# Kernel optimization log

Hardware: AMD Instinct MI355X
Metric: run time of the kernel (lower is better)

The kernel has to match this reference:

```python
import jax, jax.numpy as jnp
import numpy as np

N = 20000      # nodes
E = 160000     # edges (avg degree 16)
IN_DIM = 256
HID = 128      # hidden_dim == per-head out_channels in PyG TransformerConv
HEADS = 4
EPS = 1e-5


def setup_inputs() -> dict:
    key = jax.random.key(0)
    ks = jax.random.split(key, 24)

    def w(k, shape, scale=0.05):
        return jax.random.normal(k, shape, dtype=jnp.float32) * scale

    inp = {
        "x": jax.random.normal(ks[0], (N, IN_DIM), dtype=jnp.float32),
        "edge_index": jax.random.randint(ks[1], (2, E), 0, N, dtype=jnp.int32),
        # input projection
        "lin_w": w(ks[2], (IN_DIM, HID)), "lin_b": jnp.zeros((HID,), jnp.float32),
    }
    i = 3
    for l in (1, 2):
        inp[f"q_w{l}"] = w(ks[i], (HID, HEADS * HID)); i += 1
        inp[f"q_b{l}"] = jnp.zeros((HEADS * HID,), jnp.float32)
        inp[f"k_w{l}"] = w(ks[i], (HID, HEADS * HID)); i += 1
        inp[f"k_b{l}"] = jnp.zeros((HEADS * HID,), jnp.float32)
        inp[f"v_w{l}"] = w(ks[i], (HID, HEADS * HID)); i += 1
        inp[f"v_b{l}"] = jnp.zeros((HEADS * HID,), jnp.float32)
        inp[f"s_w{l}"] = w(ks[i], (HID, HID)); i += 1
        inp[f"s_b{l}"] = jnp.zeros((HID,), jnp.float32)
        inp[f"ln_g{l}"] = jnp.ones((HID,), jnp.float32)
        inp[f"ln_b{l}"] = jnp.zeros((HID,), jnp.float32)
    return inp


def _segment_softmax(scores, seg, num):
    # scores: [E, HEADS], seg: [E] destination indices
    m = jax.ops.segment_max(scores, seg, num_segments=num)
    m = jnp.where(jnp.isfinite(m), m, 0.0)  # guard empty segments
    e = jnp.exp(scores - m[seg])
    d = jax.ops.segment_sum(e, seg, num_segments=num)
    return e / (d[seg] + 1e-16)


def _transformer_conv(x, src, dst, qw, qb, kw, kb, vw, vb, sw, sb):
    # PyG TransformerConv(HID, HID, heads=HEADS, concat=False)
    n = x.shape[0]
    q = (x @ qw + qb).reshape(n, HEADS, HID)
    k = (x @ kw + kb).reshape(n, HEADS, HID)
    v = (x @ vw + vb).reshape(n, HEADS, HID)
    # per-edge attention: query at dst (i), key/value at src (j)
    alpha = jnp.einsum("ehd,ehd->eh", q[dst], k[src]) / jnp.sqrt(jnp.float32(HID))
    alpha = _segment_softmax(alpha, dst, n)                 # [E, HEADS]
    msg = v[src] * alpha[..., None]                          # [E, HEADS, HID]
    out = jax.ops.segment_sum(msg, dst, num_segments=n)      # [N, HEADS, HID]
    out = out.mean(axis=1)                                   # concat=False -> head mean
    return out + x @ sw + sb                                 # root skip connection


def _layer_norm(x, g, b):
    mu = x.mean(-1, keepdims=True)
    var = ((x - mu) ** 2).mean(-1, keepdims=True)
    return (x - mu) * jax.lax.rsqrt(var + EPS) * g + b


def reference(x, edge_index, lin_w, lin_b,
              q_w1, q_b1, k_w1, k_b1, v_w1, v_b1, s_w1, s_b1, ln_g1, ln_b1,
              q_w2, q_b2, k_w2, k_b2, v_w2, v_b2, s_w2, s_b2, ln_g2, ln_b2):
    src, dst = edge_index[0], edge_index[1]
    h = jax.nn.relu(x @ lin_w + lin_b)
    h1 = _transformer_conv(h, src, dst, q_w1, q_b1, k_w1, k_b1, v_w1, v_b1, s_w1, s_b1)
    h = _layer_norm(h1 + h, ln_g1, ln_b1)
    h2 = _transformer_conv(h, src, dst, q_w2, q_b2, k_w2, k_b2, v_w2, v_b2, s_w2, s_b2)
    h = _layer_norm(h2 + h, ln_g2, ln_b2)
    return h
```

## Files before the change

kernel.cpp:

```cpp
#include <hip/hip_runtime.h>
#include <math.h>

#define NNODE 20000
#define NEDGE 160000
#define IN_DIMV 256
#define HIDV 128
#define DEGCAP 64
#define RING 8

typedef __attribute__((ext_vector_type(8))) short bf16x8;
typedef __attribute__((ext_vector_type(4))) float f32x4;
typedef __attribute__((ext_vector_type(2))) float f32x2;

__device__ __forceinline__ float bf2f(unsigned short u) {
    union { unsigned int i; float f; } x; x.i = ((unsigned int)u) << 16; return x.f;
}
__device__ __forceinline__ unsigned short f2bf(float f) {
    union { float f; unsigned int i; } x; x.f = f;
    unsigned int r = x.i + 0x7fffu + ((x.i >> 16) & 1u);
    return (unsigned short)(r >> 16);
}
__device__ __forceinline__ void unpack8(uint4 p, float* f) {
    f[0] = bf2f((unsigned short)(p.x & 0xffff)); f[1] = bf2f((unsigned short)(p.x >> 16));
    f[2] = bf2f((unsigned short)(p.y & 0xffff)); f[3] = bf2f((unsigned short)(p.y >> 16));
    f[4] = bf2f((unsigned short)(p.z & 0xffff)); f[5] = bf2f((unsigned short)(p.z >> 16));
    f[6] = bf2f((unsigned short)(p.w & 0xffff)); f[7] = bf2f((unsigned short)(p.w >> 16));
}
__device__ __forceinline__ void unpack8f8_w(unsigned int a, unsigned int b, float* f) {
    f32x2 t;
    t = __builtin_amdgcn_cvt_pk_f32_fp8((int)a, false); f[0] = t.x; f[1] = t.y;
    t = __builtin_amdgcn_cvt_pk_f32_fp8((int)a, true);  f[2] = t.x; f[3] = t.y;
    t = __builtin_amdgcn_cvt_pk_f32_fp8((int)b, false); f[4] = t.x; f[5] = t.y;
    t = __builtin_amdgcn_cvt_pk_f32_fp8((int)b, true);  f[6] = t.x; f[7] = t.y;
}
__device__ __forceinline__ unsigned char f2fp8(float v) {
    int pk = __builtin_amdgcn_cvt_pk_fp8_f32(v, v, 0, false);
    return (unsigned char)(pk & 0xff);
}
__device__ __forceinline__ void gld_lds16(const unsigned short* g, unsigned short* l) {
    __builtin_amdgcn_global_load_lds((const __attribute__((address_space(1))) void*)g,
                                     (__attribute__((address_space(3))) void*)l, 16, 0, 0);
}
__device__ __forceinline__ void gld_lds16b(const unsigned char* g, unsigned char* l) {
    __builtin_amdgcn_global_load_lds((const __attribute__((address_space(1))) void*)g,
                                     (__attribute__((address_space(3))) void*)l, 16, 0, 0);
}

__global__ void convert_kernel(
    const float* __restrict__ x, const float* __restrict__ lin_w,
    const float* __restrict__ qw0, const float* __restrict__ kw0,
    const float* __restrict__ vw0, const float* __restrict__ sw0,
    const float* __restrict__ qw1, const float* __restrict__ kw1,
    const float* __restrict__ vw1, const float* __restrict__ sw1,
    unsigned short* __restrict__ xbf, unsigned short* __restrict__ arena)
{
    int idx = blockIdx.x * 256 + threadIdx.x;
    if (idx < 5120000) { xbf[idx] = f2bf(x[idx]); return; }
    int id2 = idx - 5120000;
    if (id2 >= 458752) return;
    float v;
    if (id2 < 32768) {
        int n = id2 >> 8, k = id2 & 255;
        v = lin_w[k * 128 + n];
    } else {
        int t = id2 - 32768;
        int l = t / 212992, r = t % 212992;
        int n = r >> 7, k = r & 127;
        const float* qw = l ? qw1 : qw0;
        const float* kw = l ? kw1 : kw0;
        const float* vw = l ? vw1 : vw0;
        const float* sw = l ? sw1 : sw0;
        if (n < 1536) {
            const float* w = (n < 512) ? qw : (n < 1024) ? kw : vw;
            v = w[k * 512 + (n & 511)];
        } else {
            v = sw[k * 128 + (n - 1536)];
        }
    }
    arena[id2] = f2bf(v);
}

template <int MODE, int K>
__global__ __launch_bounds__(256) void mfma_gemm(
    const unsigned short* __restrict__ A, const unsigned short* __restrict__ WT,
    const float* __restrict__ b0, const float* __restrict__ b1,
    const float* __restrict__ b2, const float* __restrict__ b3,
    unsigned short* __restrict__ qb_out, unsigned char* __restrict__ kv8_out,
    unsigned short* __restrict__ pre16_out, unsigned short* __restrict__ hbf_out)
{
    constexpr bool FULLK = (K == 128);
    __shared__ unsigned short smem[FULLK ? 32768 : 8192];
    unsigned short* ot = smem;
    unsigned char* ot8 = (unsigned char*)smem;

    int tid = threadIdx.x;
    int lane = tid & 63;
    int w = tid >> 6;
    int wm = w & 1, wn = w >> 1;
    int bm = blockIdx.x * 128;
    int bn = blockIdx.y * 128;

    int srow = lane >> 2;
    int scol = (lane & 3) * 8;
    int ar0 = bm + w * 32 + srow;      if (ar0 > NNODE - 1) ar0 = NNODE - 1;
    int ar1 = bm + w * 32 + 16 + srow; if (ar1 > NNODE - 1) ar1 = NNODE - 1;
    int br0 = bn + w * 32 + srow;
    int br1 = bn + w * 32 + 16 + srow;

    f32x4 acc[4][4] = {};
    int arow = wm * 64 + (lane & 15);
    int brow = wn * 64 + (lane & 15);
    int koff = (lane >> 4) * 8;

    if constexpr (FULLK) {
        unsigned short* As = smem;
        unsigned short* Bs = smem + 16384;
#pragma unroll
        for (int c = 0; c < 4; c++) {
            int k0 = c * 32;
            gld_lds16(A + (size_t)ar0 * K + k0 + scol, As + c * 4096 + (w * 32) * 32);
            gld_lds16(A + (size_t)ar1 * K + k0 + scol, As + c * 4096 + (w * 32 + 16) * 32);
            gld_lds16(WT + (size_t)br0 * K + k0 + scol, Bs + c * 4096 + (w * 32) * 32);
            gld_lds16(WT + (size_t)br1 * K + k0 + scol, Bs + c * 4096 + (w * 32 + 16) * 32);
        }
        __syncthreads();
#pragma unroll
        for (int c = 0; c < 4; c++) {
            bf16x8 fa[4], fb[4];
#pragma unroll
            for (int i = 0; i < 4; i++) fa[i] = *(const bf16x8*)&As[c * 4096 + (arow + i * 16) * 32 + koff];
#pragma unroll
            for (int i = 0; i < 4; i++) fb[i] = *(const bf16x8*)&Bs[c * 4096 + (brow + i * 16) * 32 + koff];
#pragma unroll
            for (int mi = 0; mi < 4; mi++)
#pragma unroll
                for (int ni = 0; ni < 4; ni++)
                    acc[mi][ni] = __builtin_amdgcn_mfma_f32_16x16x32_bf16(fa[mi], fb[ni], acc[mi][ni], 0, 0, 0);
        }
    } else {
        unsigned short* As = smem;
        unsigned short* Bs = smem + 4096;
        for (int k0 = 0; k0 < K; k0 += 32) {
            gld_lds16(A + (size_t)ar0 * K + k0 + scol, As + (w * 32) * 32);
            gld_lds16(A + (size_t)ar1 * K + k0 + scol, As + (w * 32 + 16) * 32);
            gld_lds16(WT + (size_t)br0 * K + k0 + scol, Bs + (w * 32) * 32);
            gld_lds16(WT + (size_t)br1 * K + k0 + scol, Bs + (w * 32 + 16) * 32);
            __syncthreads();
            bf16x8 fa[4], fb[4];
#pragma unroll
            for (int i = 0; i < 4; i++) fa[i] = *(const bf16x8*)&As[(arow + i * 16) * 32 + koff];
#pragma unroll
            for (int i = 0; i < 4; i++) fb[i] = *(const bf16x8*)&Bs[(brow + i * 16) * 32 + koff];
#pragma unroll
            for (int mi = 0; mi < 4; mi++)
#pragma unroll
                for (int ni = 0; ni < 4; ni++)
                    acc[mi][ni] = __builtin_amdgcn_mfma_f32_16x16x32_bf16(fa[mi], fb[ni], acc[mi][ni], 0, 0, 0);
            __syncthreads();
        }
    }

    int quad = lane >> 4, lcol = lane & 15;

    if (MODE == 1 && bn >= 512 && bn < 1536) {
        const float* bb = (bn < 1024) ? (b1 + bn - 512) : (b2 + bn - 1024);
        int coff = bn - 512;
#pragma unroll
        for (int hh = 0; hh < 2; hh++) {
            __syncthreads();
            if (wm == hh) {
#pragma unroll
                for (int mi = 0; mi < 4; mi++) {
#pragma unroll
                    for (int ni = 0; ni < 4; ni++) {
                        int lc = wn * 64 + ni * 16 + lcol;
                        float bias = bb[lc];
#pragma unroll
                        for (int reg = 0; reg < 4; reg++) {
                            int lr = mi * 16 + quad * 4 + reg;
                            ot8[lr * 128 + lc] = f2fp8(acc[mi][ni][reg] + bias);
                        }
                    }
                }
            }
            __syncthreads();
            int r = tid >> 2, ch = tid & 3;
            int row = bm + hh * 64 + r;
            if (row < NNODE) {
                uint4* dp = (uint4*)(kv8_out + (size_t)row * 1024 + coff + ch * 32);
                const uint4* sp = (const uint4*)(ot8 + r * 128 + ch * 32);
                dp[0] = sp[0];
                dp[1] = sp[1];
            }
        }
        return;
    }

    unsigned short* dst;
    int dstride, coloff;
    const float* bb;
    if (MODE == 0)           { dst = hbf_out;   dstride = HIDV; coloff = 0;  bb = b0; }
    else if (bn < 512)       { dst = qb_out;    dstride = 512;  coloff = bn; bb = b0 + bn; }
    else                     { dst = pre16_out; dstride = HIDV; coloff = 0;  bb = b3; }

#pragma unroll
    for (int hh = 0; hh < 2; hh++) {
        __syncthreads();
        if (wm == hh) {
#pragma unroll
            for (int mi = 0; mi < 4; mi++) {
#pragma unroll
                for (int ni = 0; ni < 4; ni++) {
                    int lc = wn * 64 + ni * 16 + lcol;
                    float bias = bb[lc];
#pragma unroll
                    for (int reg = 0; reg < 4; reg++) {
                        float v = acc[mi][ni][reg] + bias;
                        if (MODE == 0) v = fmaxf(v, 0.f);
                        ot[(mi * 16 + quad * 4 + reg) * 128 + lc] = f2bf(v);
                    }
                }
            }
        }
        __syncthreads();
        int r = tid >> 2, ch = tid & 3;
        int row = bm + hh * 64 + r;
        if (row < NNODE) {
            uint4* dp = (uint4*)(dst + (size_t)row * dstride + coloff + ch * 32);
            const uint4* sp = (const uint4*)(ot + r * 128 + ch * 32);
#pragma unroll
            for (int q = 0; q < 4; q++) dp[q] = sp[q];
        }
    }
}

__global__ void scatter_kernel(const int* __restrict__ ei, int* __restrict__ cursor,
                               int* __restrict__ bucket) {
    int e = blockIdx.x * blockDim.x + threadIdx.x;
    if (e < NEDGE) {
        int d = ei[NEDGE + e];
        int slot = atomicAdd(&cursor[d], 1);
        if (slot < DEGCAP) bucket[d * DEGCAP + slot] = ei[e];
    }
}

__global__ __launch_bounds__(256) void attn_ln_kernel(
    const unsigned short* __restrict__ qb, const unsigned char* __restrict__ kv8,
    const int* __restrict__ cursor, const int* __restrict__ bucket,
    const unsigned short* __restrict__ pre16, const float* __restrict__ g,
    const float* __restrict__ b,
    unsigned short* __restrict__ hbf ,
    float* __restrict__ extout)
{
    __shared__ __align__(16) unsigned char ring[4][RING * 1024];
    int lane = threadIdx.x & 63;
    int wid = threadIdx.x >> 6;
    int i = blockIdx.x * 4 + wid;
    int cnt = cursor[i]; if (cnt > DEGCAP) cnt = DEGCAP;
    const int* bk = bucket + i * DEGCAP;
    unsigned char* myring = ring[wid];

    int hg = lane >> 4;
    int sl = lane & 15;

    float qr[8];
    {
        uint4 p = *(const uint4*)(qb + (size_t)i * 512 + lane * 8);
        unpack8(p, qr);
#pragma unroll
        for (int j = 0; j < 8; j++) qr[j] *= 0.0883883476483184f;
    }

    float m = -INFINITY, l = 0.f;
    float acc[8] = {0.f, 0.f, 0.f, 0.f, 0.f, 0.f, 0.f, 0.f};

    for (int j0 = 0; j0 < cnt; j0 += RING) {
        int nb = cnt - j0; if (nb > RING) nb = RING;
        int myidx = bk[j0 + ((lane < nb) ? lane : 0)];
        asm volatile("s_waitcnt lgkmcnt(0)" ::: "memory");
#pragma unroll
        for (int t = 0; t < RING; t++) {
            if (t >= nb) break;
            int src = __shfl(myidx, t);
            gld_lds16b(kv8 + (size_t)src * 1024 + lane * 16, myring + t * 1024);
        }
        asm volatile("s_waitcnt vmcnt(0)" ::: "memory");

        float d[RING];
#pragma unroll
        for (int t = 0; t < RING; t++) d[t] = -3.0e38f;
#pragma unroll
        for (int t = 0; t < RING; t++) {
            if (t >= nb) break;
            uint2 kk = *(const uint2*)(myring + t * 1024 + hg * 128 + sl * 8);
            float kf[8];
            unpack8f8_w(kk.x, kk.y, kf);
            float s0 = qr[0] * kf[0] + qr[1] * kf[1] + qr[2] * kf[2] + qr[3] * kf[3] +
                       qr[4] * kf[4] + qr[5] * kf[5] + qr[6] * kf[6] + qr[7] * kf[7];
            d[t] = s0;
        }
#pragma unroll
        for (int t = 0; t < RING; t++) { if (t >= nb) break; d[t] += __shfl_xor(d[t], 8); }
#pragma unroll
        for (int t = 0; t < RING; t++) { if (t >= nb) break; d[t] += __shfl_xor(d[t], 4); }
#pragma unroll
        for (int t = 0; t < RING; t++) { if (t >= nb) break; d[t] += __shfl_xor(d[t], 2); }
#pragma unroll
        for (int t = 0; t < RING; t++) { if (t >= nb) break; d[t] += __shfl_xor(d[t], 1); }

        float mq = d[0];
#pragma unroll
        for (int t = 1; t < RING; t++) mq = fmaxf(mq, d[t]);
        float mn = fmaxf(m, mq);
        float scale = __expf(m - mn);
        float p[RING];
        float psum = 0.f;
#pragma unroll
        for (int t = 0; t < RING; t++) { p[t] = __expf(d[t] - mn); psum += p[t]; }
        l = l * scale + psum;
        m = mn;
#pragma unroll
        for (int c = 0; c < 8; c++) acc[c] *= scale;
#pragma unroll
        for (int t = 0; t < RING; t++) {
            if (t >= nb) break;
            uint2 vv = *(const uint2*)(myring + t * 1024 + 512 + hg * 128 + sl * 8);
            float vf[8];
            unpack8f8_w(vv.x, vv.y, vf);
            float pt = p[t];
#pragma unroll
            for (int c = 0; c < 8; c++) acc[c] += pt * vf[c];
        }
    }

    float linv = 0.25f / (l + 1e-16f);
#pragma unroll
    for (int c = 0; c < 8; c++) acc[c] *= linv;
#pragma unroll
    for (int c = 0; c < 8; c++) {
        acc[c] += __shfl_xor(acc[c], 16);
        acc[c] += __shfl_xor(acc[c], 32);
    }

    size_t base = (size_t)i * HIDV + sl * 8;
    float pv[8], hv[8];
    unpack8(*(const uint4*)(pre16 + base), pv);
    unpack8(*(const uint4*)(hbf + base), hv);
    float vals[8];
#pragma unroll
    for (int c = 0; c < 8; c++) vals[c] = acc[c] + pv[c] + hv[c];

    float s = 0.f;
#pragma unroll
    for (int c = 0; c < 8; c++) s += vals[c];
    s += __shfl_xor(s, 1); s += __shfl_xor(s, 2);
    s += __shfl_xor(s, 4); s += __shfl_xor(s, 8);
    float mu = s * (1.f / 128.f);
    float vs = 0.f;
#pragma unroll
    for (int c = 0; c < 8; c++) { float dx = vals[c] - mu; vs += dx * dx; }
    vs += __shfl_xor(vs, 1); vs += __shfl_xor(vs, 2);
    vs += __shfl_xor(vs, 4); vs += __shfl_xor(vs, 8);
    float rstd = rsqrtf(vs * (1.f / 128.f) + 1e-5f);

    float4 g0 = ((const float4*)(g + sl * 8))[0];
    float4 g1 = ((const float4*)(g + sl * 8))[1];
    float4 bb0 = ((const float4*)(b + sl * 8))[0];
    float4 bb1 = ((const float4*)(b + sl * 8))[1];
    float y[8];
    y[0] = (vals[0] - mu) * rstd * g0.x + bb0.x; y[1] = (vals[1] - mu) * rstd * g0.y + bb0.y;
    y[2] = (vals[2] - mu) * rstd * g0.z + bb0.z; y[3] = (vals[3] - mu) * rstd * g0.w + bb0.w;
    y[4] = (vals[4] - mu) * rstd * g1.x + bb1.x; y[5] = (vals[5] - mu) * rstd * g1.y + bb1.y;
    y[6] = (vals[6] - mu) * rstd * g1.z + bb1.z; y[7] = (vals[7] - mu) * rstd * g1.w + bb1.w;

    if (lane < 16) {
        unsigned short tmp[8] = {f2bf(y[0]), f2bf(y[1]), f2bf(y[2]), f2bf(y[3]),
                                 f2bf(y[4]), f2bf(y[5]), f2bf(y[6]), f2bf(y[7])};
        *(uint4*)(hbf + base) = *(uint4*)tmp;
        if (extout) {
            ((float4*)(extout + base))[0] = make_float4(y[0], y[1], y[2], y[3]);
            ((float4*)(extout + base))[1] = make_float4(y[4], y[5], y[6], y[7]);
        }
    }
}

extern "C" void kernel_launch(void* const* d_in, const int* in_sizes, int n_in,
                              void* d_out, int out_size, void* d_ws, size_t ws_size,
                              hipStream_t stream) {
    const float* x = (const float*)d_in[0];
    const int* ei = (const int*)d_in[1];

    char* ws = (char*)d_ws;
    unsigned short* hbf = (unsigned short*)(ws + 0);
    unsigned short* pre16 = (unsigned short*)(ws + 5120000);
    unsigned short* qb = (unsigned short*)(ws + 10240000);
    unsigned char* kv8 = (unsigned char*)(ws + 30720000);
    unsigned short* xbf = (unsigned short*)(ws + 51200000);
    int* cursor = (int*)(ws + 61440000);
    int* bucket = (int*)(ws + 61520000);
    unsigned short* arena = (unsigned short*)(ws + 66640000);

    convert_kernel<<<21793, 256, 0, stream>>>(
        x, (const float*)d_in[2],
        (const float*)d_in[4], (const float*)d_in[6], (const float*)d_in[8], (const float*)d_in[10],
        (const float*)d_in[14], (const float*)d_in[16], (const float*)d_in[18], (const float*)d_in[20],
        xbf, arena);

    hipMemsetAsync(cursor, 0, NNODE * sizeof(int), stream);
    scatter_kernel<<<(NEDGE + 255) / 256, 256, 0, stream>>>(ei, cursor, bucket);

    const int GM = (NNODE + 127) / 128;

    mfma_gemm<0, 256><<<dim3(GM, 1), 256, 0, stream>>>(
        xbf, arena, (const float*)d_in[3], nullptr, nullptr, nullptr,
        nullptr, nullptr, nullptr, hbf);

    for (int l = 0; l < 2; l++) {
        int o = 4 + l * 10;
        const unsigned short* WT = arena + 32768 + l * 212992;
        mfma_gemm<1, 128><<<dim3(GM, 13), 256, 0, stream>>>(
            hbf, WT,
            (const float*)d_in[o + 1], (const float*)d_in[o + 3],
            (const float*)d_in[o + 5], (const float*)d_in[o + 7],
            qb, kv8, pre16, nullptr);

        attn_ln_kernel<<<NNODE / 4, 256, 0, stream>>>(
            qb, kv8, cursor, bucket, pre16,
            (const float*)d_in[o + 8], (const float*)d_in[o + 9],
            hbf, (l == 1) ? (float*)d_out : nullptr);
    }
}
```

Before: 299.0 us.

## Reuse A tile across output panels in QKV GEMM and double-buffer attention gathers

```diff
diff --git a/kernel.cpp b/kernel.cpp
--- a/kernel.cpp
+++ b/kernel.cpp
@@ -6,7 +6,7 @@
 #define IN_DIMV 256
 #define HIDV 128
 #define DEGCAP 64
-#define RING 8
+#define BAT 4
 
 typedef __attribute__((ext_vector_type(8))) short bf16x8;
 typedef __attribute__((ext_vector_type(4))) float f32x4;
@@ -80,133 +80,152 @@
     arena[id2] = f2bf(v);
 }
 
-template <int MODE, int K>
-__global__ __launch_bounds__(256) void mfma_gemm(
+__global__ __launch_bounds__(256) void mfma_gemm0(
     const unsigned short* __restrict__ A, const unsigned short* __restrict__ WT,
-    const float* __restrict__ b0, const float* __restrict__ b1,
-    const float* __restrict__ b2, const float* __restrict__ b3,
-    unsigned short* __restrict__ qb_out, unsigned char* __restrict__ kv8_out,
-    unsigned short* __restrict__ pre16_out, unsigned short* __restrict__ hbf_out)
+    const float* __restrict__ b0, unsigned short* __restrict__ hbf_out)
 {
-    constexpr bool FULLK = (K == 128);
-    __shared__ unsigned short smem[FULLK ? 32768 : 8192];
+    __shared__ unsigned short smem[8192];
+    unsigned short* As = smem;
+    unsigned short* Bs = smem + 4096;
     unsigned short* ot = smem;
-    unsigned char* ot8 = (unsigned char*)smem;
+    const int K = 256;
 
     int tid = threadIdx.x;
     int lane = tid & 63;
     int w = tid >> 6;
     int wm = w & 1, wn = w >> 1;
     int bm = blockIdx.x * 128;
-    int bn = blockIdx.y * 128;
 
     int srow = lane >> 2;
     int scol = (lane & 3) * 8;
     int ar0 = bm + w * 32 + srow;      if (ar0 > NNODE - 1) ar0 = NNODE - 1;
     int ar1 = bm + w * 32 + 16 + srow; if (ar1 > NNODE - 1) ar1 = NNODE - 1;
-    int br0 = bn + w * 32 + srow;
-    int br1 = bn + w * 32 + 16 + srow;
+    int br0 = w * 32 + srow;
+    int br1 = w * 32 + 16 + srow;
 
     f32x4 acc[4][4] = {};
     int arow = wm * 64 + (lane & 15);
     int brow = wn * 64 + (lane & 15);
     int koff = (lane >> 4) * 8;
 
-    if constexpr (FULLK) {
-        unsigned short* As = smem;
-        unsigned short* Bs = smem + 16384;
+    for (int k0 = 0; k0 < K; k0 += 32) {
+        gld_lds16(A + (size_t)ar0 * K + k0 + scol, As + (w * 32) * 32);
+        gld_lds16(A + (size_t)ar1 * K + k0 + scol, As + (w * 32 + 16) * 32);
+        gld_lds16(WT + (size_t)br0 * K + k0 + scol, Bs + (w * 32) * 32);
+        gld_lds16(WT + (size_t)br1 * K + k0 + scol, Bs + (w * 32 + 16) * 32);
+        __syncthreads();
+        bf16x8 fa[4], fb[4];
+#pragma unroll
+        for (int i = 0; i < 4; i++) fa[i] = *(const bf16x8*)&As[(arow + i * 16) * 32 + koff];
+#pragma unroll
+        for (int i = 0; i < 4; i++) fb[i] = *(const bf16x8*)&Bs[(brow + i * 16) * 32 + koff];
+#pragma unroll
+        for (int mi = 0; mi < 4; mi++)
+#pragma unroll
+            for (int ni = 0; ni < 4; ni++)
+                acc[mi][ni] = __builtin_amdgcn_mfma_f32_16x16x32_bf16(fa[mi], fb[ni], acc[mi][ni], 0, 0, 0);
+        __syncthreads();
+    }
+
+    int quad = lane >> 4, lcol = lane & 15;
+#pragma unroll
+    for (int hh = 0; hh < 2; hh++) {
+        __syncthreads();
+        if (wm == hh) {
+#pragma unroll
+            for (int mi = 0; mi < 4; mi++) {
+#pragma unroll
+                for (int ni = 0; ni < 4; ni++) {
+                    int lc = wn * 64 + ni * 16 + lcol;
+                    float bias = b0[lc];
+#pragma unroll
+                    for (int reg = 0; reg < 4; reg++) {
+                        float v = fmaxf(acc[mi][ni][reg] + bias, 0.f);
+                        ot[(mi * 16 + quad * 4 + reg) * 128 + lc] = f2bf(v);
+                    }
+                }
+            }
+        }
+        __syncthreads();
+        int r = tid >> 2, ch = tid & 3;
+        int row = bm + hh * 64 + r;
+        if (row < NNODE) {
+            uint4* dp = (uint4*)(hbf_out + (size_t)row * HIDV + ch * 32);
+            const uint4* sp = (const uint4*)(ot + r * 128 + ch * 32);
+#pragma unroll
+            for (int q = 0; q < 4; q++) dp[q] = sp[q];
+        }
+    }
+}
+
+__global__ __launch_bounds__(256) void mfma_gemm1(
+    const unsigned short* __restrict__ A, const unsigned short* __restrict__ WT,
+    const float* __restrict__ b0, const float* __restrict__ b1,
+    const float* __restrict__ b2, const float* __restrict__ b3,
+    unsigned short* __restrict__ qb_out, unsigned char* __restrict__ kv8_out,
+    unsigned short* __restrict__ pre16_out)
+{
+    __shared__ unsigned short As[16384];
+    __shared__ unsigned short Ws[16384];
+    unsigned short* ot = Ws;
+    unsigned char* ot8 = (unsigned char*)Ws;
+    const int K = 128;
+
+    int tid = threadIdx.x;
+    int lane = tid & 63;
+    int w = tid >> 6;
+    int wm = w & 1, wn = w >> 1;
+    int bm = blockIdx.x * 128;
+    int p0 = (blockIdx.y == 0) ? 0 : 7;
+    int p1 = (blockIdx.y == 0) ? 7 : 13;
+
+    int srow = lane >> 2;
+    int scol = (lane & 3) * 8;
+    int sr0 = w * 32 + srow;
+    int sr1 = w * 32 + 16 + srow;
+    int ar0 = bm + sr0; if (ar0 > NNODE - 1) ar0 = NNODE - 1;
+    int ar1 = bm + sr1; if (ar1 > NNODE - 1) ar1 = NNODE - 1;
+
+#pragma unroll
+    for (int c = 0; c < 4; c++) {
+        int k0 = c * 32;
+        gld_lds16(A + (size_t)ar0 * K + k0 + scol, As + c * 4096 + sr0 * 32);
+        gld_lds16(A + (size_t)ar1 * K + k0 + scol, As + c * 4096 + sr1 * 32);
+    }
+
+    int arow = wm * 64 + (lane & 15);
+    int brow = wn * 64 + (lane & 15);
+    int koff = (lane >> 4) * 8;
+    int quad = lane >> 4, lcol = lane & 15;
+
+    for (int p = p0; p < p1; p++) {
+        int bn = p * 128;
 #pragma unroll
         for (int c = 0; c < 4; c++) {
             int k0 = c * 32;
-            gld_lds16(A + (size_t)ar0 * K + k0 + scol, As + c * 4096 + (w * 32) * 32);
-            gld_lds16(A + (size_t)ar1 * K + k0 + scol, As + c * 4096 + (w * 32 + 16) * 32);
-            gld_lds16(WT + (size_t)br0 * K + k0 + scol, Bs + c * 4096 + (w * 32) * 32);
-            gld_lds16(WT + (size_t)br1 * K + k0 + scol, Bs + c * 4096 + (w * 32 + 16) * 32);
-        }
-        __syncthreads();
+            gld_lds16(WT + (size_t)(bn + sr0) * K + k0 + scol, Ws + c * 4096 + sr0 * 32);
+            gld_lds16(WT + (size_t)(bn + sr1) * K + k0 + scol, Ws + c * 4096 + sr1 * 32);
+        }
+        __syncthreads();
+
+        f32x4 acc[4][4] = {};
 #pragma unroll
         for (int c = 0; c < 4; c++) {
             bf16x8 fa[4], fb[4];
 #pragma unroll
             for (int i = 0; i < 4; i++) fa[i] = *(const bf16x8*)&As[c * 4096 + (arow + i * 16) * 32 + koff];
 #pragma unroll
-            for (int i = 0; i < 4; i++) fb[i] = *(const bf16x8*)&Bs[c * 4096 + (brow + i * 16) * 32 + koff];
+            for (int i = 0; i < 4; i++) fb[i] = *(const bf16x8*)&Ws[c * 4096 + (brow + i * 16) * 32 + koff];
 #pragma unroll
             for (int mi = 0; mi < 4; mi++)
 #pragma unroll
                 for (int ni = 0; ni < 4; ni++)
                     acc[mi][ni] = __builtin_amdgcn_mfma_f32_16x16x32_bf16(fa[mi], fb[ni], acc[mi][ni], 0, 0, 0);
         }
-    } else {
-        unsigned short* As = smem;
-        unsigned short* Bs = smem + 4096;
-        for (int k0 = 0; k0 < K; k0 += 32) {
-            gld_lds16(A + (size_t)ar0 * K + k0 + scol, As + (w * 32) * 32);
-            gld_lds16(A + (size_t)ar1 * K + k0 + scol, As + (w * 32 + 16) * 32);
-            gld_lds16(WT + (size_t)br0 * K + k0 + scol, Bs + (w * 32) * 32);
-            gld_lds16(WT + (size_t)br1 * K + k0 + scol, Bs + (w * 32 + 16) * 32);
-            __syncthreads();
-            bf16x8 fa[4], fb[4];
-#pragma unroll
-            for (int i = 0; i < 4; i++) fa[i] = *(const bf16x8*)&As[(arow + i * 16) * 32 + koff];
-#pragma unroll
-            for (int i = 0; i < 4; i++) fb[i] = *(const bf16x8*)&Bs[(brow + i * 16) * 32 + koff];
-#pragma unroll
-            for (int mi = 0; mi < 4; mi++)
-#pragma unroll
-                for (int ni = 0; ni < 4; ni++)
-                    acc[mi][ni] = __builtin_amdgcn_mfma_f32_16x16x32_bf16(fa[mi], fb[ni], acc[mi][ni], 0, 0, 0);
-            __syncthreads();
-        }
-    }
-
-    int quad = lane >> 4, lcol = lane & 15;
-
-    if (MODE == 1 && bn >= 512 && bn < 1536) {
-        const float* bb = (bn < 1024) ? (b1 + bn - 512) : (b2 + bn - 1024);
-        int coff = bn - 512;
-#pragma unroll
-        for (int hh = 0; hh < 2; hh++) {
-            __syncthreads();
-            if (wm == hh) {
-#pragma unroll
-                for (int mi = 0; mi < 4; mi++) {
-#pragma unroll
-                    for (int ni = 0; ni < 4; ni++) {
-                        int lc = wn * 64 + ni * 16 + lcol;
-                        float bias = bb[lc];
-#pragma unroll
-                        for (int reg = 0; reg < 4; reg++) {
-                            int lr = mi * 16 + quad * 4 + reg;
-                            ot8[lr * 128 + lc] = f2fp8(acc[mi][ni][reg] + bias);
-                        }
-                    }
-                }
-            }
-            __syncthreads();
-            int r = tid >> 2, ch = tid & 3;
-            int row = bm + hh * 64 + r;
-            if (row < NNODE) {
-                uint4* dp = (uint4*)(kv8_out + (size_t)row * 1024 + coff + ch * 32);
-                const uint4* sp = (const uint4*)(ot8 + r * 128 + ch * 32);
-                dp[0] = sp[0];
-                dp[1] = sp[1];
-            }
-        }
-        return;
-    }
-
-    unsigned short* dst;
-    int dstride, coloff;
-    const float* bb;
-    if (MODE == 0)           { dst = hbf_out;   dstride = HIDV; coloff = 0;  bb = b0; }
-    else if (bn < 512)       { dst = qb_out;    dstride = 512;  coloff = bn; bb = b0 + bn; }
-    else                     { dst = pre16_out; dstride = HIDV; coloff = 0;  bb = b3; }
-
-#pragma unroll
-    for (int hh = 0; hh < 2; hh++) {
-        __syncthreads();
-        if (wm == hh) {
+        __syncthreads();
+
+        if (p < 4 || p == 12) {
+            const float* bb = (p < 4) ? (b0 + bn) : b3;
 #pragma unroll
             for (int mi = 0; mi < 4; mi++) {
 #pragma unroll
@@ -214,22 +233,46 @@
                     int lc = wn * 64 + ni * 16 + lcol;
                     float bias = bb[lc];
 #pragma unroll
-                    for (int reg = 0; reg < 4; reg++) {
-                        float v = acc[mi][ni][reg] + bias;
-                        if (MODE == 0) v = fmaxf(v, 0.f);
-                        ot[(mi * 16 + quad * 4 + reg) * 128 + lc] = f2bf(v);
-                    }
+                    for (int reg = 0; reg < 4; reg++)
+                        ot[(wm * 64 + mi * 16 + quad * 4 + reg) * 128 + lc] = f2bf(acc[mi][ni][reg] + bias);
                 }
             }
-        }
-        __syncthreads();
-        int r = tid >> 2, ch = tid & 3;
-        int row = bm + hh * 64 + r;
-        if (row < NNODE) {
-            uint4* dp = (uint4*)(dst + (size_t)row * dstride + coloff + ch * 32);
-            const uint4* sp = (const uint4*)(ot + r * 128 + ch * 32);
-#pragma unroll
-            for (int q = 0; q < 4; q++) dp[q] = sp[q];
+            __syncthreads();
+            int r = tid >> 1, hf = tid & 1;
+            int row = bm + r;
+            if (row < NNODE) {
+                unsigned short* dst = (p < 4) ? (qb_out + (size_t)row * 512 + bn + hf * 64)
+                                              : (pre16_out + (size_t)row * HIDV + hf * 64);
+                const uint4* sp = (const uint4*)(ot + r * 128 + hf * 64);
+                uint4* dp = (uint4*)dst;
+#pragma unroll
+                for (int q = 0; q < 8; q++) dp[q] = sp[q];
+            }
+            __syncthreads();
+        } else {
+            const float* bb = (bn < 1024) ? (b1 + bn - 512) : (b2 + bn - 1024);
+            int coff = bn - 512;
+#pragma unroll
+            for (int mi = 0; mi < 4; mi++) {
+#pragma unroll
+                for (int ni = 0; ni < 4; ni++) {
+                    int lc = wn * 64 + ni * 16 + lcol;
+                    float bias = bb[lc];
+#pragma unroll
+                    for (int reg = 0; reg < 4; reg++)
+                        ot8[(wm * 64 + mi * 16 + quad * 4 + reg) * 128 + lc] = f2fp8(acc[mi][ni][reg] + bias);
+                }
+            }
+            __syncthreads();
+            int r = tid >> 1, hf = tid & 1;
+            int row = bm + r;
+            if (row < NNODE) {
+                uint4* dp = (uint4*)(kv8_out + (size_t)row * 1024 + coff + hf * 64);
+                const uint4* sp = (const uint4*)(ot8 + r * 128 + hf * 64);
+#pragma unroll
+                for (int q = 0; q < 4; q++) dp[q] = sp[q];
+            }
+            __syncthreads();
         }
     }
 }
@@ -252,13 +295,12 @@
     unsigned short* __restrict__ hbf ,
     float* __restrict__ extout)
 {
-    __shared__ __align__(16) unsigned char ring[4][RING * 1024];
+    __shared__ __align__(16) unsigned char ring[4][2][BAT * 1024];
     int lane = threadIdx.x & 63;
     int wid = threadIdx.x >> 6;
     int i = blockIdx.x * 4 + wid;
     int cnt = cursor[i]; if (cnt > DEGCAP) cnt = DEGCAP;
     const int* bk = bucket + i * DEGCAP;
-    unsigned char* myring = ring[wid];
 
     int hg = lane >> 4;
     int sl = lane & 15;
@@ -274,62 +316,76 @@
     float m = -INFINITY, l = 0.f;
     float acc[8] = {0.f, 0.f, 0.f, 0.f, 0.f, 0.f, 0.f, 0.f};
 
-    for (int j0 = 0; j0 < cnt; j0 += RING) {
-        int nb = cnt - j0; if (nb > RING) nb = RING;
-        int myidx = bk[j0 + ((lane < nb) ? lane : 0)];
-        asm volatile("s_waitcnt lgkmcnt(0)" ::: "memory");
-#pragma unroll
-        for (int t = 0; t < RING; t++) {
-            if (t >= nb) break;
-            int src = __shfl(myidx, t);
-            gld_lds16b(kv8 + (size_t)src * 1024 + lane * 16, myring + t * 1024);
-        }
-        asm volatile("s_waitcnt vmcnt(0)" ::: "memory");
-
-        float d[RING];
-#pragma unroll
-        for (int t = 0; t < RING; t++) d[t] = -3.0e38f;
-#pragma unroll
-        for (int t = 0; t < RING; t++) {
-            if (t >= nb) break;
-            uint2 kk = *(const uint2*)(myring + t * 1024 + hg * 128 + sl * 8);
-            float kf[8];
-            unpack8f8_w(kk.x, kk.y, kf);
-            float s0 = qr[0] * kf[0] + qr[1] * kf[1] + qr[2] * kf[2] + qr[3] * kf[3] +
+    if (cnt > 0) {
+        int myidx = bk[(lane < cnt) ? lane : 0];
+
+        auto issue = [&](int bb, unsigned char* half) {
+#pragma unroll
+            for (int t = 0; t < BAT; t++) {
+                int j = bb * BAT + t; if (j >= cnt) j = cnt - 1;
+                int src = __shfl(myidx, j);
+                gld_lds16b(kv8 + (size_t)src * 1024 + lane * 16, half + t * 1024);
+            }
+        };
+
+        issue(0, ring[wid][0]);
+        for (int bb = 0; bb * BAT < cnt; bb++) {
+            unsigned char* cur = ring[wid][bb & 1];
+            unsigned char* nxt = ring[wid][(bb + 1) & 1];
+            bool more = (bb + 1) * BAT < cnt;
+            if (more) {
+                asm volatile("s_waitcnt lgkmcnt(0)" ::: "memory");
+                issue(bb + 1, nxt);
+                asm volatile("s_waitcnt vmcnt(4)" ::: "memory");
+            } else {
+                asm volatile("s_waitcnt vmcnt(0)" ::: "memory");
+            }
+            int rem = cnt - bb * BAT;
+
+            float d[BAT];
+#pragma unroll
+            for (int t = 0; t < BAT; t++) d[t] = -3.0e38f;
+#pragma unroll
+            for (int t = 0; t < BAT; t++) {
+                if (t >= rem) break;
+                uint2 kk = *(const uint2*)(cur + t * 1024 + hg * 128 + sl * 8);
+                float kf[8];
+                unpack8f8_w(kk.x, kk.y, kf);
+                d[t] = qr[0] * kf[0] + qr[1] * kf[1] + qr[2] * kf[2] + qr[3] * kf[3] +
                        qr[4] * kf[4] + qr[5] * kf[5] + qr[6] * kf[6] + qr[7] * kf[7];
-            d[t] = s0;
-        }
-#pragma unroll
-        for (int t = 0; t < RING; t++) { if (t >= nb) break; d[t] += __shfl_xor(d[t], 8); }
-#pragma unroll
-        for (int t = 0; t < RING; t++) { if (t >= nb) break; d[t] += __shfl_xor(d[t], 4); }
-#pragma unroll
-        for (int t = 0; t < RING; t++) { if (t >= nb) break; d[t] += __shfl_xor(d[t], 2); }
-#pragma unroll
-        for (int t = 0; t < RING; t++) { if (t >= nb) break; d[t] += __shfl_xor(d[t], 1); }
-
-        float mq = d[0];
-#pragma unroll
-        for (int t = 1; t < RING; t++) mq = fmaxf(mq, d[t]);
-        float mn = fmaxf(m, mq);
-        float scale = __expf(m - mn);
-        float p[RING];
-        float psum = 0.f;
-#pragma unroll
-        for (int t = 0; t < RING; t++) { p[t] = __expf(d[t] - mn); psum += p[t]; }
-        l = l * scale + psum;
-        m = mn;
-#pragma unroll
-        for (int c = 0; c < 8; c++) acc[c] *= scale;
-#pragma unroll
-        for (int t = 0; t < RING; t++) {
-            if (t >= nb) break;
-            uint2 vv = *(const uint2*)(myring + t * 1024 + 512 + hg * 128 + sl * 8);
-            float vf[8];
-            unpack8f8_w(vv.x, vv.y, vf);
-            float pt = p[t];
-#pragma unroll
-            for (int c = 0; c < 8; c++) acc[c] += pt * vf[c];
+            }
+#pragma unroll
+            for (int t = 0; t < BAT; t++) { if (t >= rem) break; d[t] += __shfl_xor(d[t], 8); }
+#pragma unroll
+            for (int t = 0; t < BAT; t++) { if (t >= rem) break; d[t] += __shfl_xor(d[t], 4); }
+#pragma unroll
+            for (int t = 0; t < BAT; t++) { if (t >= rem) break; d[t] += __shfl_xor(d[t], 2); }
+#pragma unroll
+            for (int t = 0; t < BAT; t++) { if (t >= rem) break; d[t] += __shfl_xor(d[t], 1); }
+
+            float mq = d[0];
+#pragma unroll
+            for (int t = 1; t < BAT; t++) mq = fmaxf(mq, d[t]);
+            float mn = fmaxf(m, mq);
+            float scale = __expf(m - mn);
+            float p[BAT];
+            float psum = 0.f;
+#pragma unroll
+            for (int t = 0; t < BAT; t++) { p[t] = __expf(d[t] - mn); psum += p[t]; }
+            l = l * scale + psum;
+            m = mn;
+#pragma unroll
+            for (int c = 0; c < 8; c++) acc[c] *= scale;
+#pragma unroll
+            for (int t = 0; t < BAT; t++) {
+                if (t >= rem) break;
+                uint2 vv = *(const uint2*)(cur + t * 1024 + 512 + hg * 128 + sl * 8);
+                float vf[8];
+                unpack8f8_w(vv.x, vv.y, vf);
+                float pt = p[t];
+#pragma unroll
+                for (int c = 0; c < 8; c++) acc[c] += pt * vf[c];
+            }
         }
     }
 
@@ -411,18 +467,16 @@
 
     const int GM = (NNODE + 127) / 128;
 
-    mfma_gemm<0, 256><<<dim3(GM, 1), 256, 0, stream>>>(
-        xbf, arena, (const float*)d_in[3], nullptr, nullptr, nullptr,
-        nullptr, nullptr, nullptr, hbf);
+    mfma_gemm0<<<GM, 256, 0, stream>>>(xbf, arena, (const float*)d_in[3], hbf);
 
     for (int l = 0; l < 2; l++) {
         int o = 4 + l * 10;
         const unsigned short* WT = arena + 32768 + l * 212992;
-        mfma_gemm<1, 128><<<dim3(GM, 13), 256, 0, stream>>>(
+        mfma_gemm1<<<dim3(GM, 2), 256, 0, stream>>>(
             hbf, WT,
             (const float*)d_in[o + 1], (const float*)d_in[o + 3],
             (const float*)d_in[o + 5], (const float*)d_in[o + 7],
-            qb, kv8, pre16, nullptr);
+            qb, kv8, pre16);
 
         attn_ln_kernel<<<NNODE / 4, 256, 0, stream>>>(
             qb, kv8, cursor, bucket, pre16,
```

Result: no change. 296.3 us (-0.9%).
